# Optimization experiments

Measured on AMD Instinct MI355X. Metric: run time of the kernel, lower is better.

## Reference

```python
import jax, jax.numpy as jnp
import numpy as np

B, T, C = 2, 2048, 1024
H = 16
D = C // H  # head_size = 64
EPS = 1e-5


def setup_inputs() -> dict:
    key = jax.random.key(0)
    ks = jax.random.split(key, 16)
    s = lambda fan_in: fan_in ** -0.5
    return {
        "x": jax.random.normal(ks[0], (B, T, C), jnp.float32),
        "Wq": jax.random.normal(ks[1], (H, C, D), jnp.float32) * s(C),
        "Wk": jax.random.normal(ks[2], (H, C, D), jnp.float32) * s(C),
        "Wv": jax.random.normal(ks[3], (H, C, D), jnp.float32) * s(C),
        "Wproj": jax.random.normal(ks[4], (C, C), jnp.float32) * s(C),
        "bproj": jnp.zeros((C,), jnp.float32),
        "W1": jax.random.normal(ks[5], (C, 4 * C), jnp.float32) * s(C),
        "b1": jnp.zeros((4 * C,), jnp.float32),
        "W2": jax.random.normal(ks[6], (4 * C, C), jnp.float32) * s(4 * C),
        "b2": jnp.zeros((C,), jnp.float32),
        "ln1_g": jnp.ones((C,), jnp.float32),
        "ln1_b": jnp.zeros((C,), jnp.float32),
        "ln2_g": jnp.ones((C,), jnp.float32),
        "ln2_b": jnp.zeros((C,), jnp.float32),
    }


def _layernorm(x, g, b):
    mu = jnp.mean(x, axis=-1, keepdims=True)
    var = jnp.mean(jnp.square(x - mu), axis=-1, keepdims=True)
    return (x - mu) * jax.lax.rsqrt(var + EPS) * g + b


def _block(x, Wq, Wk, Wv, Wproj, bproj, W1, b1, W2, b2,
           ln1_g, ln1_b, ln2_g, ln2_b):
    # --- multi-head causal self-attention (pre-LN) ---
    h = _layernorm(x, ln1_g, ln1_b)
    q = jnp.einsum("btc,hcd->bhtd", h, Wq)
    k = jnp.einsum("btc,hcd->bhtd", h, Wk)
    v = jnp.einsum("btc,hcd->bhtd", h, Wv)
    scores = jnp.einsum("bhtd,bhsd->bhts", q, k) * (D ** -0.5)  # [B,H,T,T]
    causal = jnp.tril(jnp.ones((T, T), bool))
    scores = jnp.where(causal, scores, -jnp.inf)
    att = jax.nn.softmax(scores, axis=-1)
    out = jnp.einsum("bhts,bhsd->bhtd", att, v)  # [B,H,T,D]
    out = out.transpose(0, 2, 1, 3).reshape(B, T, H * D)  # concat heads
    x = x + out @ Wproj + bproj
    # --- feed-forward ---
    h2 = _layernorm(x, ln2_g, ln2_b)
    ff = jax.nn.relu(h2 @ W1 + b1) @ W2 + b2
    return x + ff


def reference(x, Wq, Wk, Wv, Wproj, bproj, W1, b1, W2, b2,
              ln1_g, ln1_b, ln2_g, ln2_b):
    return _block(x, Wq, Wk, Wv, Wproj, bproj, W1, b1, W2, b2,
                  ln1_g, ln1_b, ln2_g, ln2_b)
```

## Files before the change

### kernel.cpp

```cpp
#include <hip/hip_runtime.h>

typedef __bf16 bf16x8 __attribute__((ext_vector_type(8)));
typedef float  f32x4  __attribute__((ext_vector_type(4)));

union U8 { bf16x8 v; __bf16 e[8]; unsigned short u[8]; };

__device__ __forceinline__ unsigned short f2bf(float f) {
  unsigned int u = __float_as_uint(f);
  unsigned int r = (u + 0x7FFFu + ((u >> 16) & 1u)) >> 16;
  return (unsigned short)r;
}

__device__ __forceinline__ void async16(const void* g, void* l) {
  __builtin_amdgcn_global_load_lds(
      (__attribute__((address_space(1))) void*)(g),
      (__attribute__((address_space(3))) void*)(l), 16, 0, 0);
}

__device__ __forceinline__ void block_barrier() {
  asm volatile("" ::: "memory");
  __builtin_amdgcn_sched_barrier(0);
  __builtin_amdgcn_s_barrier();
  __builtin_amdgcn_sched_barrier(0);
  asm volatile("" ::: "memory");
}

__global__ __launch_bounds__(256) void transpose_w(
    const float* __restrict__ in, unsigned short* __restrict__ out,
    int R, int Cc) {
  __shared__ float tile[32][33];
  const int batch = blockIdx.z;
  const float* ip = in + (size_t)batch * R * Cc;
  unsigned short* op = out + (size_t)batch * R * Cc;
  const int c0 = blockIdx.x * 32, r0 = blockIdx.y * 32;
  const int tx = threadIdx.x, ty = threadIdx.y;
#pragma unroll
  for (int i = 0; i < 32; i += 8)
    tile[ty + i][tx] = ip[(size_t)(r0 + ty + i) * Cc + c0 + tx];
  __syncthreads();
#pragma unroll
  for (int i = 0; i < 32; i += 8)
    op[(size_t)(c0 + ty + i) * R + r0 + tx] = f2bf(tile[tx][ty + i]);
}

__global__ __launch_bounds__(256) void ln_kernel(
    const float* __restrict__ x, const float* __restrict__ g,
    const float* __restrict__ bta, unsigned short* __restrict__ out) {
  const int C = 1024;
  const int row = blockIdx.x, tid = threadIdx.x;
  const float4 v = ((const float4*)(x + (size_t)row * C))[tid];
  float s  = v.x + v.y + v.z + v.w;
  float ss = v.x * v.x + v.y * v.y + v.z * v.z + v.w * v.w;
#pragma unroll
  for (int off = 32; off > 0; off >>= 1) {
    s  += __shfl_down(s, off);
    ss += __shfl_down(ss, off);
  }
  __shared__ float r0[4], r1[4];
  const int wave = tid >> 6, lane = tid & 63;
  if (lane == 0) { r0[wave] = s; r1[wave] = ss; }
  __syncthreads();
  s  = r0[0] + r0[1] + r0[2] + r0[3];
  ss = r1[0] + r1[1] + r1[2] + r1[3];
  const float mu   = s * (1.0f / C);
  const float var  = ss * (1.0f / C) - mu * mu;
  const float rstd = rsqrtf(var + 1e-5f);
  const float4 gv = ((const float4*)g)[tid];
  const float4 bv = ((const float4*)bta)[tid];
  ushort4 o;
  o.x = f2bf((v.x - mu) * rstd * gv.x + bv.x);
  o.y = f2bf((v.y - mu) * rstd * gv.y + bv.y);
  o.z = f2bf((v.z - mu) * rstd * gv.z + bv.z);
  o.w = f2bf((v.w - mu) * rstd * gv.w + bv.w);
  ((ushort4*)(out + (size_t)row * C))[tid] = o;
}

__global__ __launch_bounds__(256, 2) void gemm_lat2(
    const unsigned short* __restrict__ A, const unsigned short* __restrict__ BT,
    float* __restrict__ Cout, const float* __restrict__ bias,
    const float* __restrict__ resid, int M, int N, int K) {
  __shared__ __align__(16) unsigned short As[3][8192];
  __shared__ __align__(16) unsigned short Bs[3][4096];
  const int tid = threadIdx.x;
  const int lane = tid & 63, wave = tid >> 6;
  const int wm = wave >> 1, wn = wave & 1;
  const int lr = lane & 15, lg = lane >> 4;

  const int nwg = gridDim.x;
  const int cpx = nwg >> 3;
  const int swz = ((int)blockIdx.x & 7) * cpx + ((int)blockIdx.x >> 3);
  const int Nt = N >> 6;
  const int g4 = swz / (4 * Nt);
  const int rem = swz - g4 * 4 * Nt;
  const int m0 = (g4 * 4 + (rem & 3)) << 7;
  const int n0 = (rem >> 2) << 6;

  const int srow = tid >> 3;
  const int sc = ((tid & 7) ^ (srow & 7)) << 3;
  const unsigned short* Ag = A + (size_t)(m0 + srow) * K + sc;
  const unsigned short* Bg = BT + (size_t)(n0 + srow) * K + sc;
  const size_t rskip = (size_t)32 * K;

  f32x4 acc[4][2] = {};
  const int nkt = K >> 6;

#define STG(T, B)                                                          \
  {                                                                        \
    const int kt_ = (T) << 6;                                              \
    _Pragma("unroll")                                                      \
    for (int j = 0; j < 4; ++j)                                            \
      async16(Ag + kt_ + (size_t)j * rskip, &As[B][j * 2048 + tid * 8]);   \
    async16(Bg + kt_, &Bs[B][tid * 8]);                                    \
    async16(Bg + kt_ + rskip, &Bs[B][2048 + tid * 8]);                     \
  }

  STG(0, 0);
  STG(1, 1);

  for (int t = 0; t < nkt; ++t) {
    const int buf = t % 3;
    if (t + 1 < nkt) asm volatile("s_waitcnt vmcnt(6)" ::: "memory");
    else             asm volatile("s_waitcnt vmcnt(0)" ::: "memory");
    block_barrier();
    if (t + 2 < nkt) {
      int sb = buf + 2; if (sb >= 3) sb -= 3;
      STG(t + 2, sb);
    }
#pragma unroll
    for (int kh = 0; kh < 2; ++kh) {
      const int kc = ((kh * 4 + lg) ^ (lr & 7)) << 3;
      bf16x8 afr[4], bfr[2];
#pragma unroll
      for (int fm = 0; fm < 4; fm++)
        afr[fm] = *(const bf16x8*)&As[buf][(wm * 64 + fm * 16 + lr) * 64 + kc];
#pragma unroll
      for (int fn = 0; fn < 2; fn++)
        bfr[fn] = *(const bf16x8*)&Bs[buf][(wn * 32 + fn * 16 + lr) * 64 + kc];
#pragma unroll
      for (int fm = 0; fm < 4; fm++)
#pragma unroll
        for (int fn = 0; fn < 2; fn++)
          acc[fm][fn] = __builtin_amdgcn_mfma_f32_16x16x32_bf16(
              afr[fm], bfr[fn], acc[fm][fn], 0, 0, 0);
    }
  }
#undef STG

#pragma unroll
  for (int fn = 0; fn < 2; fn++) {
    const int col = n0 + wn * 32 + fn * 16 + lr;
    const float bv = bias[col];
#pragma unroll
    for (int fm = 0; fm < 4; fm++) {
      const int row0 = m0 + wm * 64 + fm * 16 + lg * 4;
#pragma unroll
      for (int r = 0; r < 4; r++) {
        const size_t idx = (size_t)(row0 + r) * N + col;
        Cout[idx] = acc[fm][fn][r] + bv + resid[idx];
      }
    }
  }
}

template <int EPI>
__global__ __launch_bounds__(512, 2) void gemm8p(
    const unsigned short* __restrict__ A, const unsigned short* __restrict__ BT,
    void* __restrict__ Cout, void* __restrict__ Cout2,
    const float* __restrict__ bias, int M, int N, int K) {
  __shared__ __align__(16) unsigned short As[2][2][8192];
  __shared__ __align__(16) unsigned short Bs[2][2][8192];
  const int tid = threadIdx.x;
  const int lane = tid & 63;
  const int wave = tid >> 6;
  const int wm = wave >> 2, wn = wave & 3;
  const int lr = lane & 15, lg = lane >> 4;

  const int nwg = gridDim.x;
  const int cpx = nwg >> 3;
  const int swz = ((int)blockIdx.x & 7) * cpx + ((int)blockIdx.x >> 3);
  const int Nt = N >> 8;
  const int g4 = swz / (4 * Nt);
  const int rem = swz - g4 * 4 * Nt;
  const int m0 = (g4 * 4 + (rem & 3)) << 8;
  const int n0 = (rem >> 2) << 8;

  const int srow = tid >> 2;
  const int scg = ((tid & 3) ^ ((srow >> 1) & 3)) << 3;
  const unsigned short* Ag = A + (size_t)(m0 + srow) * K + scg;
  const unsigned short* Bg = BT + (size_t)(n0 + srow) * K + scg;
  const size_t rskip = (size_t)128 * K;
  const int l8 = tid * 8;

  const int kch = (lg ^ ((lr >> 1) & 3)) << 3;

  f32x4 acc[8][4] = {};
  bf16x8 afr[4], bfr[4];
  const int nkt = K >> 6;

  async16(Ag, &As[0][0][l8]);            async16(Ag + rskip, &As[0][0][l8 + 4096]);
  async16(Bg, &Bs[0][0][l8]);            async16(Bg + rskip, &Bs[0][0][l8 + 4096]);
  async16(Ag + 32, &As[0][1][l8]);       async16(Ag + 32 + rskip, &As[0][1][l8 + 4096]);
  async16(Bg + 32, &Bs[0][1][l8]);       async16(Bg + 32 + rskip, &Bs[0][1][l8 + 4096]);
  async16(Ag + 64, &As[1][0][l8]);       async16(Ag + 64 + rskip, &As[1][0][l8 + 4096]);
  async16(Bg + 64, &Bs[1][0][l8]);       async16(Bg + 64 + rskip, &Bs[1][0][l8 + 4096]);
  asm volatile("s_waitcnt vmcnt(4)" ::: "memory");
  block_barrier();

  for (int t = 0; t < nkt; ++t) {
    const int buf = t & 1, nbuf = buf ^ 1;
    const int kt1 = (t + 1) << 6, kt2 = (t + 2) << 6;
    const bool s1 = (t + 1 < nkt), s2 = (t + 2 < nkt);

#pragma unroll
    for (int fm = 0; fm < 4; fm++)
      afr[fm] = *(const bf16x8*)&As[buf][0][(wm * 128 + fm * 16 + lr) * 32 + kch];
#pragma unroll
    for (int fn = 0; fn < 4; fn++)
      bfr[fn] = *(const bf16x8*)&Bs[buf][0][(wn * 64 + fn * 16 + lr) * 32 + kch];
    if (s1) {
      async16(Ag + kt1 + 32, &As[nbuf][1][l8]);
      async16(Ag + kt1 + 32 + rskip, &As[nbuf][1][l8 + 4096]);
    }
    block_barrier();
    __builtin_amdgcn_s_setprio(1);
#pragma unroll
    for (int fm = 0; fm < 4; fm++)
#pragma unroll
      for (int fn = 0; fn < 4; fn++)
        acc[fm][fn] = __builtin_amdgcn_mfma_f32_16x16x32_bf16(afr[fm], bfr[fn], acc[fm][fn], 0, 0, 0);
    __builtin_amdgcn_s_setprio(0);
    block_barrier();

#pragma unroll
    for (int fm = 0; fm < 4; fm++)
      afr[fm] = *(const bf16x8*)&As[buf][0][(wm * 128 + 64 + fm * 16 + lr) * 32 + kch];
    if (s1) {
      async16(Bg + kt1 + 32, &Bs[nbuf][1][l8]);
      async16(Bg + kt1 + 32 + rskip, &Bs[nbuf][1][l8 + 4096]);
    }
    block_barrier();
    __builtin_amdgcn_s_setprio(1);
#pragma unroll
    for (int fm = 0; fm < 4; fm++)
#pragma unroll
      for (int fn = 0; fn < 4; fn++)
        acc[4 + fm][fn] = __builtin_amdgcn_mfma_f32_16x16x32_bf16(afr[fm], bfr[fn], acc[4 + fm][fn], 0, 0, 0);
    __builtin_amdgcn_s_setprio(0);
    block_barrier();

#pragma unroll
    for (int fm = 0; fm < 4; fm++)
      afr[fm] = *(const bf16x8*)&As[buf][1][(wm * 128 + fm * 16 + lr) * 32 + kch];
#pragma unroll
    for (int fn = 0; fn < 4; fn++)
      bfr[fn] = *(const bf16x8*)&Bs[buf][1][(wn * 64 + fn * 16 + lr) * 32 + kch];
    if (s2) {
      async16(Ag + kt2, &As[buf][0][l8]);
      async16(Ag + kt2 + rskip, &As[buf][0][l8 + 4096]);
    }
    block_barrier();
    __builtin_amdgcn_s_setprio(1);
#pragma unroll
    for (int fm = 0; fm < 4; fm++)
#pragma unroll
      for (int fn = 0; fn < 4; fn++)
        acc[fm][fn] = __builtin_amdgcn_mfma_f32_16x16x32_bf16(afr[fm], bfr[fn], acc[fm][fn], 0, 0, 0);
    __builtin_amdgcn_s_setprio(0);
    block_barrier();

#pragma unroll
    for (int fm = 0; fm < 4; fm++)
      afr[fm] = *(const bf16x8*)&As[buf][1][(wm * 128 + 64 + fm * 16 + lr) * 32 + kch];
    if (s2) {
      async16(Bg + kt2, &Bs[buf][0][l8]);
      async16(Bg + kt2 + rskip, &Bs[buf][0][l8 + 4096]);
    }
    block_barrier();
    __builtin_amdgcn_s_setprio(1);
#pragma unroll
    for (int fm = 0; fm < 4; fm++)
#pragma unroll
      for (int fn = 0; fn < 4; fn++)
        acc[4 + fm][fn] = __builtin_amdgcn_mfma_f32_16x16x32_bf16(afr[fm], bfr[fn], acc[4 + fm][fn], 0, 0, 0);
    __builtin_amdgcn_s_setprio(0);
    if (s2) asm volatile("s_waitcnt vmcnt(4)" ::: "memory");
    else    asm volatile("s_waitcnt vmcnt(0)" ::: "memory");
    block_barrier();
  }

#pragma unroll
  for (int fn = 0; fn < 4; fn++) {
    const int col = n0 + wn * 64 + fn * 16 + lr;
    float bv = 0.0f;
    if (EPI == 2) bv = bias[col];
#pragma unroll
    for (int fm = 0; fm < 8; fm++) {
      const int row0 = m0 + wm * 128 + fm * 16 + lg * 4;
      if (EPI == 2) {
#pragma unroll
        for (int r = 0; r < 4; r++)
          ((unsigned short*)Cout)[(size_t)(row0 + r) * N + col] =
              f2bf(fmaxf(acc[fm][fn][r] + bv, 0.0f));
      } else {
        if (col < 2048) {
#pragma unroll
          for (int r = 0; r < 4; r++)
            ((unsigned short*)Cout)[(size_t)(row0 + r) * 2048 + col] =
                f2bf(acc[fm][fn][r]);
        } else {
          ushort4 ov;
          ov.x = f2bf(acc[fm][fn][0]);
          ov.y = f2bf(acc[fm][fn][1]);
          ov.z = f2bf(acc[fm][fn][2]);
          ov.w = f2bf(acc[fm][fn][3]);
          *(ushort4*)((unsigned short*)Cout2 + (size_t)(col - 2048) * 4096 + row0) = ov;
        }
      }
    }
  }
}

__global__ __launch_bounds__(256) void attn_kernel(
    const unsigned short* __restrict__ qk, const unsigned short* __restrict__ vT,
    unsigned short* __restrict__ o) {
  const int T = 2048, C = 1024, QKS = 2048;
  const int tid = threadIdx.x;
  const int wave = tid >> 6, lane = tid & 63;
  const int lr = lane & 15, lg = lane >> 4;
  const int b = blockIdx.y >> 4, hh = blockIdx.y & 15;
  const size_t rowb = (size_t)b * T * QKS;
  const int qcol = hh * 64;
  const int kcol = 1024 + hh * 64;
  const int vrow0 = hh * 64;
  const size_t bT = (size_t)b * T;
  const int swe = (lr & 7) << 3;

  __shared__ __align__(16) unsigned short Ks[2][64 * 64];
  __shared__ __align__(16) unsigned short Vs[2][64 * 64];
  __shared__ __align__(16) unsigned short Ps[4][16][72];

  const int rw = tid >> 3;
  const int c8 = ((tid & 7) ^ (rw & 7)) << 3;

#pragma unroll 1
  for (int pass = 0; pass < 2; ++pass) {
    const int qt = (pass == 0) ? (int)blockIdx.x : (31 - (int)blockIdx.x);
    const int qbase = qt * 64 + wave * 16;
    const int trow = qbase + lr;

    U8 qf[2];
#pragma unroll
    for (int j = 0; j < 2; j++)
      qf[j].v = *(const bf16x8*)(qk + rowb + (size_t)trow * QKS + qcol + j * 32 + lg * 8);
    asm volatile("s_waitcnt vmcnt(0)" ::: "memory");

    async16(qk + rowb + (size_t)rw * QKS + kcol + c8, Ks[0] + tid * 8);
    async16(qk + rowb + (size_t)(32 + rw) * QKS + kcol + c8, Ks[0] + 2048 + tid * 8);
    async16(vT + (size_t)(vrow0 + rw) * 4096 + bT + c8, Vs[0] + tid * 8);
    async16(vT + (size_t)(vrow0 + 32 + rw) * 4096 + bT + c8, Vs[0] + 2048 + tid * 8);

    f32x4 oa[4] = {};
    float mrun = -1e30f, lsum = 0.0f;
    int cur = 0;

    for (int sb = 0; sb <= qt; ++sb) {
      if (sb < qt) {
        const int s1 = (sb + 1) * 64;
        const int nb = cur ^ 1;
        async16(qk + rowb + (size_t)(s1 + rw) * QKS + kcol + c8, Ks[nb] + tid * 8);
        async16(qk + rowb + (size_t)(s1 + 32 + rw) * QKS + kcol + c8, Ks[nb] + 2048 + tid * 8);
        async16(vT + (size_t)(vrow0 + rw) * 4096 + bT + s1 + c8, Vs[nb] + tid * 8);
        async16(vT + (size_t)(vrow0 + 32 + rw) * 4096 + bT + s1 + c8, Vs[nb] + 2048 + tid * 8);
        asm volatile("s_waitcnt vmcnt(4)" ::: "memory");
      } else {
        asm volatile("s_waitcnt vmcnt(0)" ::: "memory");
      }
      block_barrier();

      const unsigned short* Kc = Ks[cur];
      const unsigned short* Vc = Vs[cur];
      const int s0 = sb * 64;

      f32x4 sa[4] = {};
#pragma unroll
      for (int j = 0; j < 2; j++) {
#pragma unroll
        for (int mf = 0; mf < 4; mf++) {
          U8 kf;
          kf.v = *(const bf16x8*)(Kc + (mf * 16 + lr) * 64 + ((j * 32 + lg * 8) ^ swe));
          sa[mf] = __builtin_amdgcn_mfma_f32_16x16x32_bf16(kf.v, qf[j].v, sa[mf], 0, 0, 0);
        }
      }
      float sv[16];
#pragma unroll
      for (int mf = 0; mf < 4; mf++)
#pragma unroll
        for (int r = 0; r < 4; r++) sv[mf * 4 + r] = sa[mf][r] * 0.125f;

      if (sb == qt) {
#pragma unroll
        for (int mf = 0; mf < 4; mf++)
#pragma unroll
          for (int r = 0; r < 4; r++)
            if (s0 + mf * 16 + lg * 4 + r > trow) sv[mf * 4 + r] = -1e30f;
      }

      float tm = sv[0];
#pragma unroll
      for (int i = 1; i < 16; i++) tm = fmaxf(tm, sv[i]);
      tm = fmaxf(tm, __shfl_xor(tm, 16));
      tm = fmaxf(tm, __shfl_xor(tm, 32));

      if (!__all(tm <= mrun + 8.0f)) {
        const float mn = fmaxf(mrun, tm);
        const float corr = __expf(mrun - mn);
        lsum *= corr;
#pragma unroll
        for (int c = 0; c < 4; c++)
#pragma unroll
          for (int r = 0; r < 4; r++) oa[c][r] *= corr;
        mrun = mn;
      }

      float rs = 0.0f;
#pragma unroll
      for (int i = 0; i < 16; i++) {
        sv[i] = __expf(sv[i] - mrun);
        rs += sv[i];
      }
      rs += __shfl_xor(rs, 16);
      rs += __shfl_xor(rs, 32);
      lsum += rs;

#pragma unroll
      for (int mf = 0; mf < 4; mf++) {
        ushort4 w;
        w.x = f2bf(sv[mf * 4 + 0]);
        w.y = f2bf(sv[mf * 4 + 1]);
        w.z = f2bf(sv[mf * 4 + 2]);
        w.w = f2bf(sv[mf * 4 + 3]);
        *(ushort4*)&Ps[wave][lr][mf * 16 + lg * 4] = w;
      }
      asm volatile("" ::: "memory");
      U8 pb[2];
      pb[0].v = *(const bf16x8*)&Ps[wave][lr][lg * 8];
      pb[1].v = *(const bf16x8*)&Ps[wave][lr][32 + lg * 8];
      asm volatile("" ::: "memory");

#pragma unroll
      for (int c = 0; c < 4; c++) {
#pragma unroll
        for (int ks = 0; ks < 2; ks++) {
          U8 vf;
          vf.v = *(const bf16x8*)(Vc + (c * 16 + lr) * 64 + ((ks * 32 + lg * 8) ^ swe));
          oa[c] = __builtin_amdgcn_mfma_f32_16x16x32_bf16(vf.v, pb[ks].v, oa[c], 0, 0, 0);
        }
      }

      block_barrier();
      cur ^= 1;
    }

    const float inv = 1.0f / lsum;
#pragma unroll
    for (int c = 0; c < 4; c++) {
      ushort4 ov;
      ov.x = f2bf(oa[c][0] * inv);
      ov.y = f2bf(oa[c][1] * inv);
      ov.z = f2bf(oa[c][2] * inv);
      ov.w = f2bf(oa[c][3] * inv);
      *(ushort4*)(o + (size_t)(bT + trow) * C + hh * 64 + c * 16 + lg * 4) = ov;
    }
  }
}

extern "C" void kernel_launch(void* const* d_in, const int* in_sizes, int n_in,
                              void* d_out, int out_size, void* d_ws, size_t ws_size,
                              hipStream_t stream) {
  (void)in_sizes; (void)n_in; (void)out_size; (void)ws_size;
  const int T = 2048, C = 1024, M = 2 * T, C4 = 4 * C;

  const float* x     = (const float*)d_in[0];
  const float* Wq    = (const float*)d_in[1];
  const float* Wk    = (const float*)d_in[2];
  const float* Wv    = (const float*)d_in[3];
  const float* Wproj = (const float*)d_in[4];
  const float* bproj = (const float*)d_in[5];
  const float* W1    = (const float*)d_in[6];
  const float* b1    = (const float*)d_in[7];
  const float* W2    = (const float*)d_in[8];
  const float* b2    = (const float*)d_in[9];
  const float* ln1g  = (const float*)d_in[10];
  const float* ln1b  = (const float*)d_in[11];
  const float* ln2g  = (const float*)d_in[12];
  const float* ln2b  = (const float*)d_in[13];
  float* out = (float*)d_out;

  char* ws = (char*)d_ws;
  const size_t MBy = (size_t)1 << 20;
  unsigned short* WqkvT = (unsigned short*)(ws + 0 * MBy);
  unsigned short* WqT = WqkvT;
  unsigned short* WkT = WqkvT + 1024 * 1024;
  unsigned short* WvT = WqkvT + 2048 * 1024;
  unsigned short* WpT = (unsigned short*)(ws + 6 * MBy);
  unsigned short* W1T = (unsigned short*)(ws + 8 * MBy);
  unsigned short* W2T = (unsigned short*)(ws + 16 * MBy);
  unsigned short* h   = (unsigned short*)(ws + 24 * MBy);
  unsigned short* qkb = (unsigned short*)(ws + 32 * MBy);
  unsigned short* vTb = (unsigned short*)(ws + 48 * MBy);
  unsigned short* att = (unsigned short*)(ws + 56 * MBy);
  float*          x1  = (float*)(ws + 64 * MBy);
  unsigned short* h2  = att;
  unsigned short* ff1 = h;

  const dim3 tb(32, 8);
  transpose_w<<<dim3(2, 32, 16), tb, 0, stream>>>(Wq, WqT, 1024, 64);
  transpose_w<<<dim3(2, 32, 16), tb, 0, stream>>>(Wk, WkT, 1024, 64);
  transpose_w<<<dim3(2, 32, 16), tb, 0, stream>>>(Wv, WvT, 1024, 64);
  transpose_w<<<dim3(32, 32, 1), tb, 0, stream>>>(Wproj, WpT, 1024, 1024);
  transpose_w<<<dim3(128, 32, 1), tb, 0, stream>>>(W1, W1T, 1024, 4096);
  transpose_w<<<dim3(32, 128, 1), tb, 0, stream>>>(W2, W2T, 4096, 1024);

  ln_kernel<<<M, 256, 0, stream>>>(x, ln1g, ln1b, h);

  gemm8p<4><<<192, 512, 0, stream>>>(h, WqkvT, qkb, vTb, nullptr, M, 3072, C);

  attn_kernel<<<dim3(16, 32), 256, 0, stream>>>(qkb, vTb, att);

  gemm_lat2<<<512, 256, 0, stream>>>(att, WpT, x1, bproj, x, M, C, C);

  ln_kernel<<<M, 256, 0, stream>>>(x1, ln2g, ln2b, h2);

  gemm8p<2><<<256, 512, 0, stream>>>(h2, W1T, ff1, nullptr, b1, M, C4, C);

  gemm_lat2<<<512, 256, 0, stream>>>(ff1, W2T, out, b2, x1, M, C, C4);
}
```

Measured before the change: 252.2 us.

## Split-K the FFN down-projection, fold softmax scale into Q, use exp2

```diff
diff --git a/kernel.cpp b/kernel.cpp
--- a/kernel.cpp
+++ b/kernel.cpp
@@ -6,9 +6,9 @@
 union U8 { bf16x8 v; __bf16 e[8]; unsigned short u[8]; };
 
 __device__ __forceinline__ unsigned short f2bf(float f) {
-  unsigned int u = __float_as_uint(f);
-  unsigned int r = (u + 0x7FFFu + ((u >> 16) & 1u)) >> 16;
-  return (unsigned short)r;
+  union { __bf16 b; unsigned short u; } c;
+  c.b = (__bf16)f;
+  return c.u;
 }
 
 __device__ __forceinline__ void async16(const void* g, void* l) {
@@ -162,7 +162,29 @@
   }
 }
 
-template <int EPI>
+__global__ __launch_bounds__(256) void reduce_add4(
+    const unsigned short* __restrict__ p01, const unsigned short* __restrict__ p23,
+    const float* __restrict__ bias, float* __restrict__ out, int n4) {
+  const int stride = gridDim.x * 256;
+#define BF(u) __uint_as_float(((unsigned)(u)) << 16)
+  for (int i = blockIdx.x * 256 + threadIdx.x; i < n4; i += stride) {
+    const ushort4 a = ((const ushort4*)p01)[i];
+    const ushort4 b = ((const ushort4*)p01)[i + n4];
+    const ushort4 c = ((const ushort4*)p23)[i];
+    const ushort4 d = ((const ushort4*)p23)[i + n4];
+    const float4 r = ((const float4*)out)[i];
+    const float4 bv = ((const float4*)bias)[i & 255];
+    float4 o;
+    o.x = (BF(a.x) + BF(b.x)) + (BF(c.x) + BF(d.x)) + r.x + bv.x;
+    o.y = (BF(a.y) + BF(b.y)) + (BF(c.y) + BF(d.y)) + r.y + bv.y;
+    o.z = (BF(a.z) + BF(b.z)) + (BF(c.z) + BF(d.z)) + r.z + bv.z;
+    o.w = (BF(a.w) + BF(b.w)) + (BF(c.w) + BF(d.w)) + r.w + bv.w;
+    ((float4*)out)[i] = o;
+  }
+#undef BF
+}
+
+template <int EPI, int SPLITK>
 __global__ __launch_bounds__(512, 2) void gemm8p(
     const unsigned short* __restrict__ A, const unsigned short* __restrict__ BT,
     void* __restrict__ Cout, void* __restrict__ Cout2,
@@ -178,16 +200,24 @@
   const int nwg = gridDim.x;
   const int cpx = nwg >> 3;
   const int swz = ((int)blockIdx.x & 7) * cpx + ((int)blockIdx.x >> 3);
+  int tile = swz, ks = 0;
+  if (SPLITK > 1) {
+    const int tilesPer = nwg / SPLITK;
+    ks = swz / tilesPer;
+    tile = swz - ks * tilesPer;
+  }
+  const int Ksl = K / SPLITK;
+  const int k0 = ks * Ksl;
   const int Nt = N >> 8;
-  const int g4 = swz / (4 * Nt);
-  const int rem = swz - g4 * 4 * Nt;
+  const int g4 = tile / (4 * Nt);
+  const int rem = tile - g4 * 4 * Nt;
   const int m0 = (g4 * 4 + (rem & 3)) << 8;
   const int n0 = (rem >> 2) << 8;
 
   const int srow = tid >> 2;
   const int scg = ((tid & 3) ^ ((srow >> 1) & 3)) << 3;
-  const unsigned short* Ag = A + (size_t)(m0 + srow) * K + scg;
-  const unsigned short* Bg = BT + (size_t)(n0 + srow) * K + scg;
+  const unsigned short* Ag = A + (size_t)(m0 + srow) * K + k0 + scg;
+  const unsigned short* Bg = BT + (size_t)(n0 + srow) * K + k0 + scg;
   const size_t rskip = (size_t)128 * K;
   const int l8 = tid * 8;
 
@@ -195,7 +225,7 @@
 
   f32x4 acc[8][4] = {};
   bf16x8 afr[4], bfr[4];
-  const int nkt = K >> 6;
+  const int nkt = Ksl >> 6;
 
   async16(Ag, &As[0][0][l8]);            async16(Ag + rskip, &As[0][0][l8 + 4096]);
   async16(Bg, &Bs[0][0][l8]);            async16(Bg + rskip, &Bs[0][0][l8 + 4096]);
@@ -301,12 +331,20 @@
         for (int r = 0; r < 4; r++)
           ((unsigned short*)Cout)[(size_t)(row0 + r) * N + col] =
               f2bf(fmaxf(acc[fm][fn][r] + bv, 0.0f));
+      } else if (EPI == 5) {
+        unsigned short* P = (unsigned short*)(ks < 2 ? Cout : Cout2) +
+                            (size_t)(ks & 1) * M * N;
+#pragma unroll
+        for (int r = 0; r < 4; r++)
+          P[(size_t)(row0 + r) * N + col] = f2bf(acc[fm][fn][r]);
       } else {
         if (col < 2048) {
 #pragma unroll
-          for (int r = 0; r < 4; r++)
-            ((unsigned short*)Cout)[(size_t)(row0 + r) * 2048 + col] =
-                f2bf(acc[fm][fn][r]);
+          for (int r = 0; r < 4; r++) {
+            float val = acc[fm][fn][r];
+            if (col < 1024) val *= 0.18033688011112042f;
+            ((unsigned short*)Cout)[(size_t)(row0 + r) * 2048 + col] = f2bf(val);
+          }
         } else {
           ushort4 ov;
           ov.x = f2bf(acc[fm][fn][0]);
@@ -395,7 +433,7 @@
 #pragma unroll
       for (int mf = 0; mf < 4; mf++)
 #pragma unroll
-        for (int r = 0; r < 4; r++) sv[mf * 4 + r] = sa[mf][r] * 0.125f;
+        for (int r = 0; r < 4; r++) sv[mf * 4 + r] = sa[mf][r];
 
       if (sb == qt) {
 #pragma unroll
@@ -405,15 +443,18 @@
             if (s0 + mf * 16 + lg * 4 + r > trow) sv[mf * 4 + r] = -1e30f;
       }
 
-      float tm = sv[0];
-#pragma unroll
-      for (int i = 1; i < 16; i++) tm = fmaxf(tm, sv[i]);
+      float t8[8];
+#pragma unroll
+      for (int i = 0; i < 8; i++) t8[i] = fmaxf(sv[i], sv[i + 8]);
+#pragma unroll
+      for (int i = 0; i < 4; i++) t8[i] = fmaxf(t8[i], t8[i + 4]);
+      float tm = fmaxf(fmaxf(t8[0], t8[1]), fmaxf(t8[2], t8[3]));
       tm = fmaxf(tm, __shfl_xor(tm, 16));
       tm = fmaxf(tm, __shfl_xor(tm, 32));
 
       if (!__all(tm <= mrun + 8.0f)) {
         const float mn = fmaxf(mrun, tm);
-        const float corr = __expf(mrun - mn);
+        const float corr = __builtin_amdgcn_exp2f(mrun - mn);
         lsum *= corr;
 #pragma unroll
         for (int c = 0; c < 4; c++)
@@ -422,12 +463,15 @@
         mrun = mn;
       }
 
-      float rs = 0.0f;
-#pragma unroll
-      for (int i = 0; i < 16; i++) {
-        sv[i] = __expf(sv[i] - mrun);
-        rs += sv[i];
-      }
+#pragma unroll
+      for (int i = 0; i < 16; i++)
+        sv[i] = __builtin_amdgcn_exp2f(sv[i] - mrun);
+      float s8[8];
+#pragma unroll
+      for (int i = 0; i < 8; i++) s8[i] = sv[i] + sv[i + 8];
+#pragma unroll
+      for (int i = 0; i < 4; i++) s8[i] = s8[i] + s8[i + 4];
+      float rs = (s8[0] + s8[1]) + (s8[2] + s8[3]);
       rs += __shfl_xor(rs, 16);
       rs += __shfl_xor(rs, 32);
       lsum += rs;
@@ -509,9 +553,11 @@
   unsigned short* qkb = (unsigned short*)(ws + 32 * MBy);
   unsigned short* vTb = (unsigned short*)(ws + 48 * MBy);
   unsigned short* att = (unsigned short*)(ws + 56 * MBy);
-  float*          x1  = (float*)(ws + 64 * MBy);
+  float* x1 = out;
   unsigned short* h2  = att;
   unsigned short* ff1 = h;
+  unsigned short* ffP01 = (unsigned short*)(ws + 0 * MBy);
+  unsigned short* ffP23 = (unsigned short*)(ws + 64 * MBy);
 
   const dim3 tb(32, 8);
   transpose_w<<<dim3(2, 32, 16), tb, 0, stream>>>(Wq, WqT, 1024, 64);
@@ -523,7 +569,7 @@
 
   ln_kernel<<<M, 256, 0, stream>>>(x, ln1g, ln1b, h);
 
-  gemm8p<4><<<192, 512, 0, stream>>>(h, WqkvT, qkb, vTb, nullptr, M, 3072, C);
+  gemm8p<4, 1><<<192, 512, 0, stream>>>(h, WqkvT, qkb, vTb, nullptr, M, 3072, C);
 
   attn_kernel<<<dim3(16, 32), 256, 0, stream>>>(qkb, vTb, att);
 
@@ -531,7 +577,8 @@
 
   ln_kernel<<<M, 256, 0, stream>>>(x1, ln2g, ln2b, h2);
 
-  gemm8p<2><<<256, 512, 0, stream>>>(h2, W1T, ff1, nullptr, b1, M, C4, C);
-
-  gemm_lat2<<<512, 256, 0, stream>>>(ff1, W2T, out, b2, x1, M, C, C4);
-}
+  gemm8p<2, 1><<<256, 512, 0, stream>>>(h2, W1T, ff1, nullptr, b1, M, C4, C);
+
+  gemm8p<5, 4><<<256, 512, 0, stream>>>(ff1, W2T, ffP01, ffP23, nullptr, M, C, C4);
+  reduce_add4<<<2048, 256, 0, stream>>>(ffP01, ffP23, b2, out, M * C / 4);
+}
```

New measurement: 243.5 us. 3.4% less time.
